# Kernel tuning notes

Measured on AMD Instinct MI355X. Metric: run time of the kernel, lower is better.

Reference implementation:

```python
import jax, jax.numpy as jnp
import numpy as np

B_, L_, DM = 64, 2048, 12
DI, DS, DC, DTR = 24, 16, 4, 1  # d_inner=expand*d_model, d_state, d_conv, dt_rank=ceil(12/16)


def _ln(x, g, b, eps=1e-12):
    m = x.mean(-1, keepdims=True)
    v = ((x - m) ** 2).mean(-1, keepdims=True)
    return (x - m) / jnp.sqrt(v + eps) * g + b


def setup_inputs() -> dict:
    key = jax.random.key(0)
    ks = jax.random.split(key, 16)
    r = lambda k, s, sc=0.1: jax.random.normal(k, s, jnp.float32) * sc
    A = jnp.tile(jnp.arange(1, DS + 1, dtype=jnp.float32), (DI, 1))  # standard S4D-real init
    return {
        "x": jax.random.normal(ks[0], (B_, L_, DM), jnp.float32),
        "in_proj_w": r(ks[1], (2 * DI, DM)),
        "conv_w": r(ks[2], (DI, 1, DC)),
        "conv_b": r(ks[3], (DI,)),
        "x_proj_w": r(ks[4], (DTR + 2 * DS, DI)),
        "dt_w": r(ks[5], (DI, DTR)),
        "dt_b": r(ks[6], (DI,)),
        "A_log": jnp.log(A),
        "Dp": r(ks[7], (DI,)) + 1.0,
        "out_proj_w": r(ks[8], (DM, DI)),
        "ln1_g": jnp.ones(DM, jnp.float32), "ln1_b": jnp.zeros(DM, jnp.float32),
        "ffn_w1": r(ks[9], (4 * DM, DM)), "ffn_b1": jnp.zeros(4 * DM, jnp.float32),
        "ffn_w2": r(ks[10], (DM, 4 * DM)), "ffn_b2": jnp.zeros(DM, jnp.float32),
        "ffn_ln_g": jnp.ones(DM, jnp.float32), "ffn_ln_b": jnp.zeros(DM, jnp.float32),
        "cnn_w": r(ks[11], (DM, DM, 3)), "cnn_b": r(ks[12], (DM,)),
        "lin1_w": r(ks[13], (12, 24)), "lin1_b": jnp.zeros(12, jnp.float32),
        "lin2_w": r(ks[14], (20, 12)), "lin2_b": jnp.zeros(20, jnp.float32),
        "lin3_w": r(ks[15], (1, 20)), "lin3_b": jnp.zeros(1, jnp.float32),
    }


def reference(x, in_proj_w, conv_w, conv_b, x_proj_w, dt_w, dt_b, A_log, Dp,
              out_proj_w, ln1_g, ln1_b, ffn_w1, ffn_b1, ffn_w2, ffn_b2,
              ffn_ln_g, ffn_ln_b, cnn_w, cnn_b, lin1_w, lin1_b,
              lin2_w, lin2_b, lin3_w, lin3_b):
    Bsz = x.shape[0]
    # ---- Mamba block ----
    xz = jnp.einsum('bld,ed->ble', x, in_proj_w)            # [B,L,2*DI]
    xi, z = xz[..., :DI], xz[..., DI:]
    xc = jax.lax.conv_general_dilated(
        xi.transpose(0, 2, 1), conv_w, (1,), [(DC - 1, 0)],
        dimension_numbers=('NCH', 'OIH', 'NCH'), feature_group_count=DI)
    xi = jax.nn.silu(xc.transpose(0, 2, 1) + conv_b)        # causal depthwise conv + SiLU
    xdb = jnp.einsum('bld,ed->ble', xi, x_proj_w)           # [B,L,dt_rank+2*DS]
    dt, Bm, Cm = xdb[..., :DTR], xdb[..., DTR:DTR + DS], xdb[..., DTR + DS:]
    delta = jax.nn.softplus(jnp.einsum('blr,dr->bld', dt, dt_w) + dt_b)  # [B,L,DI]
    A = -jnp.exp(A_log)                                     # [DI,DS]
    dA = jnp.exp(delta[..., None] * A)                      # [B,L,DI,DS]
    dBx = delta[..., None] * Bm[:, :, None, :] * xi[..., None]

    def step(h, inp):
        a, bx, c = inp
        h = a * h + bx                                      # [B,DI,DS]
        return h, jnp.einsum('bdn,bn->bd', h, c)

    h0 = jnp.zeros((Bsz, DI, DS), x.dtype)
    _, ys = jax.lax.scan(step, h0, (dA.transpose(1, 0, 2, 3),
                                    dBx.transpose(1, 0, 2, 3),
                                    Cm.transpose(1, 0, 2)))
    y = ys.transpose(1, 0, 2) + xi * Dp                     # skip D*x
    y = y * jax.nn.silu(z)
    m_out = jnp.einsum('ble,de->bld', y, out_proj_w)        # [B,L,DM]
    h = _ln(m_out, ln1_g, ln1_b)                            # num_layers==1: no residual
    # ---- FeedForward (with residual + LN) ----
    ff = jax.nn.gelu(jnp.einsum('bld,ed->ble', h, ffn_w1) + ffn_b1, approximate=False)
    ff = jnp.einsum('ble,de->bld', ff, ffn_w2) + ffn_b2
    x_mamba = _ln(ff + h, ffn_ln_g, ffn_ln_b)
    # ---- FFT magnitude + Conv1d path (padding=1 to keep length L; see notes) ----
    xf = jnp.abs(jnp.fft.fft(x, axis=1)).astype(x.dtype)
    xcnn = jax.lax.conv_general_dilated(
        xf.transpose(0, 2, 1), cnn_w, (1,), [(1, 1)],
        dimension_numbers=('NCH', 'OIH', 'NCH')) + cnn_b[None, :, None]
    xcnn = xcnn.transpose(0, 2, 1)                          # [B,L,12]
    # ---- fusion head ----
    comb = jnp.concatenate([x_mamba, xcnn], axis=-1)        # [B,L,24]
    o = jax.nn.elu(jnp.einsum('ble,de->bld', comb, lin1_w) + lin1_b)
    o = jnp.einsum('bld,ed->ble', o, lin2_w) + lin2_b
    o = jnp.einsum('ble,oe->blo', o, lin3_w) + lin3_b       # [B,L,1]
    return jax.nn.sigmoid(o.mean(axis=1)).squeeze()          # [B]
```

## Files before the change

### kernel.cpp

```cpp
#include <hip/hip_runtime.h>
#include <math.h>

#define B_  64
#define L_  2048
#define DM  12
#define DI  24
#define DS  16
#define DC  4
#define DTR 1
#define T_  (B_ * L_)
#define NCHUNK 128
#define CHUNK  16


__device__ __forceinline__ float siluf(float v)  { return v / (1.0f + __expf(-v)); }
__device__ __forceinline__ float eluf(float v) { return v > 0.0f ? v : __expf(v) - 1.0f; }

__device__ __forceinline__ float fast_erff(float x) {
    const float ax = fabsf(x);
    const float t  = 1.0f / fmaf(0.3275911f, ax, 1.0f);
    float p = fmaf(1.061405429f, t, -1.453152027f);
    p = fmaf(p, t, 1.421413741f);
    p = fmaf(p, t, -0.284496736f);
    p = fmaf(p, t, 0.254829592f);
    p *= t;
    const float r = 1.0f - p * __expf(-ax * ax);
    return copysignf(r, x);
}
__device__ __forceinline__ float geluf(float v) {
    return 0.5f * v * (1.0f + fast_erff(v * 0.70710678118654752440f));
}

__global__ __launch_bounds__(256) void k_proj_fft(
    const float* __restrict__ x, const float* __restrict__ w_in,
    const float* __restrict__ conv_w, const float* __restrict__ conv_b,
    const float* __restrict__ xproj_w,
    float* __restrict__ xi_out, float* __restrict__ zs_out,
    float* __restrict__ dt_out, float* __restrict__ Bm_out,
    float* __restrict__ Cm_out, float* __restrict__ xfT)
{
    __shared__ float smem[12620];
    const int tid = threadIdx.x;

    if (blockIdx.x < 512) {
        float* s_st = smem + 6476;
        const int b   = blockIdx.x >> 3;
        const int l0  = (blockIdx.x & 7) << 8;
        const int l   = l0 + tid;
        const int t   = b * L_ + l;
        const size_t t0 = (size_t)b * L_ + l0;

        float xv[DM];
        *(float4*)&xv[0] = *(const float4*)&x[t * DM + 0];
        *(float4*)&xv[4] = *(const float4*)&x[t * DM + 4];
        *(float4*)&xv[8] = *(const float4*)&x[t * DM + 8];

        float zsv[DI];
#pragma unroll
        for (int e = 0; e < DI; ++e) {
            float acc = 0.0f, accz = 0.0f;
#pragma unroll
            for (int d = 0; d < DM; ++d) {
                acc  += xv[d] * w_in[e * DM + d];
                accz += xv[d] * w_in[(DI + e) * DM + d];
            }
            smem[(tid + 3) * 25 + e] = acc;
            zsv[e] = siluf(accz);
        }
        if (tid < 3) {
            const int lh = l0 - 3 + tid;
            if (lh < 0) {
                for (int e = 0; e < DI; ++e) smem[tid * 25 + e] = 0.0f;
            } else {
                const int th = b * L_ + lh;
                float xh[DM];
                for (int d = 0; d < DM; ++d) xh[d] = x[th * DM + d];
                for (int e = 0; e < DI; ++e) {
                    float acc = 0.0f;
                    for (int d = 0; d < DM; ++d) acc += xh[d] * w_in[e * DM + d];
                    smem[tid * 25 + e] = acc;
                }
            }
        }
#pragma unroll
        for (int e = 0; e < DI; ++e) s_st[tid * DI + e] = zsv[e];
        __syncthreads();
        {
            float4* g = (float4*)(zs_out + t0 * DI);
            const float4* s4 = (const float4*)s_st;
#pragma unroll
            for (int k = 0; k < 6; ++k) g[k * 256 + tid] = s4[k * 256 + tid];
        }

        float xi[DI];
#pragma unroll
        for (int dch = 0; dch < DI; ++dch) {
            float acc = conv_b[dch];
#pragma unroll
            for (int k = 0; k < DC; ++k)
                acc += smem[(tid + k) * 25 + dch] * conv_w[dch * DC + k];
            xi[dch] = siluf(acc);
        }
        float dt = 0.0f;
#pragma unroll
        for (int d = 0; d < DI; ++d) dt += xi[d] * xproj_w[d];
        dt_out[t] = dt;
        float Bv[DS], Cv[DS];
#pragma unroll
        for (int e = 0; e < DS; ++e) {
            float accB = 0.0f, accC = 0.0f;
#pragma unroll
            for (int d = 0; d < DI; ++d) {
                accB += xi[d] * xproj_w[(1 + e) * DI + d];
                accC += xi[d] * xproj_w[(1 + DS + e) * DI + d];
            }
            Bv[e] = accB;
            Cv[e] = accC;
        }

        __syncthreads();
#pragma unroll
        for (int e = 0; e < DI; ++e) s_st[tid * DI + e] = xi[e];
        __syncthreads();
        {
            float4* g = (float4*)(xi_out + t0 * DI);
            const float4* s4 = (const float4*)s_st;
#pragma unroll
            for (int k = 0; k < 6; ++k) g[k * 256 + tid] = s4[k * 256 + tid];
        }
        __syncthreads();
#pragma unroll
        for (int e = 0; e < DS; ++e) s_st[tid * DS + e] = Bv[e];
        __syncthreads();
        {
            float4* g = (float4*)(Bm_out + t0 * DS);
            const float4* s4 = (const float4*)s_st;
#pragma unroll
            for (int k = 0; k < 4; ++k) g[k * 256 + tid] = s4[k * 256 + tid];
        }
        __syncthreads();
#pragma unroll
        for (int e = 0; e < DS; ++e) s_st[tid * DS + e] = Cv[e];
        __syncthreads();
        {
            float4* g = (float4*)(Cm_out + t0 * DS);
            const float4* s4 = (const float4*)s_st;
#pragma unroll
            for (int k = 0; k < 4; ++k) g[k * 256 + tid] = s4[k * 256 + tid];
        }
    } else {
        float* re  = smem;
        float* im  = smem + 2048;
        float* twr = smem + 4096;
        float* twi = smem + 5120;
        const int bid = blockIdx.x - 512;
        const int b   = bid / (DM / 2);
        const int p   = bid % (DM / 2);
        for (int j = tid; j < 1024; j += 256) {
            const float ang = -6.283185307179586f * (float)j * (1.0f / 2048.0f);
            float s, c;
            sincosf(ang, &s, &c);
            twr[j] = c; twi[j] = s;
        }
        for (int i = tid; i < 2048; i += 256) {
            const int r = (int)(__brev((unsigned)i) >> 21);
            const float2 v = *(const float2*)&x[(size_t)(b * L_ + i) * DM + 2 * p];
            re[r] = v.x;
            im[r] = v.y;
        }
        __syncthreads();
        for (int s = 1; s <= 11; ++s) {
            const int half  = 1 << (s - 1);
            const int tstep = 2048 >> s;
            for (int i = tid; i < 1024; i += 256) {
                const int j   = i & (half - 1);
                const int grp = i >> (s - 1);
                const int pos = (grp << s) + j;
                const float wr = twr[j * tstep], wi = twi[j * tstep];
                const float ar = re[pos + half], ai = im[pos + half];
                const float vr = wr * ar - wi * ai;
                const float vi = wr * ai + wi * ar;
                const float ur = re[pos], ui = im[pos];
                re[pos] = ur + vr;          im[pos] = ui + vi;
                re[pos + half] = ur - vr;   im[pos + half] = ui - vi;
            }
            __syncthreads();
        }
        float* row1 = xfT + (size_t)(b * DM + 2 * p) * L_;
        float* row2 = row1 + L_;
        for (int k = tid; k < 2048; k += 256) {
            const int nk = (2048 - k) & 2047;
            const float zr = re[k],  zi = im[k];
            const float qr = re[nk], qi = im[nk];
            const float e1r = zr + qr, e1i = zi - qi;
            const float e2r = zr - qr, e2i = zi + qi;
            row1[k] = 0.5f * sqrtf(e1r * e1r + e1i * e1i);
            row2[k] = 0.5f * sqrtf(e2r * e2r + e2i * e2i);
        }
    }
}

__global__ __launch_bounds__(384) void k_scan1(
    const float* __restrict__ dt_in, const float* __restrict__ xi,
    const float* __restrict__ Bm, const float* __restrict__ A_log,
    const float* __restrict__ dt_w, const float* __restrict__ dt_b,
    float* __restrict__ Sd, float* __restrict__ H)
{
    const int tid = threadIdx.x;
    const int d   = tid % DI;
    const int cl  = tid / DI;
    const int b   = blockIdx.x >> 3;
    const int c   = ((blockIdx.x & 7) << 4) + cl;
    const int t0  = b * L_ + c * CHUNK;

    float An[DS];
#pragma unroll
    for (int j = 0; j < DS; ++j) An[j] = -__expf(A_log[d * DS + j]);
    const float dtw = dt_w[d], dtb = dt_b[d];

    float h[DS];
#pragma unroll
    for (int j = 0; j < DS; ++j) h[j] = 0.0f;
    float sumdel = 0.0f;

    const float*  pDt = dt_in + t0;
    const float*  pX  = xi + (size_t)t0 * DI + d;
    const float4* pB  = (const float4*)(Bm + (size_t)t0 * DS);

#pragma unroll 4
    for (int i = 0; i < CHUNK; ++i) {
        const float v = fmaf(pDt[i], dtw, dtb);
        const float e = __expf(v);
        const float delta = (v > 20.0f) ? v : __logf(1.0f + e);
        const float u = delta * pX[i * DI];
        sumdel += delta;
        const float4 B0 = pB[i * 4 + 0];
        const float4 B1 = pB[i * 4 + 1];
        const float4 B2 = pB[i * 4 + 2];
        const float4 B3 = pB[i * 4 + 3];
#pragma unroll
        for (int j = 0; j < DS; ++j) {
            const float a = __expf(delta * An[j]);
            h[j] = a * h[j] + u * ((j < 4) ? (&B0.x)[j] : (j < 8) ? (&B1.x)[j - 4]
                                   : (j < 12) ? (&B2.x)[j - 8] : (&B3.x)[j - 12]);
        }
    }
    const int cu = (b * DI + d) * NCHUNK + c;
    Sd[cu] = sumdel;
    float4* pH = (float4*)(H + (size_t)cu * DS);
    pH[0] = make_float4(h[0], h[1], h[2], h[3]);
    pH[1] = make_float4(h[4], h[5], h[6], h[7]);
    pH[2] = make_float4(h[8], h[9], h[10], h[11]);
    pH[3] = make_float4(h[12], h[13], h[14], h[15]);
}

__global__ __launch_bounds__(256) void k_scan2(
    const float* __restrict__ Sd, float* __restrict__ H,
    const float* __restrict__ A_log)
{
    const int idx  = blockIdx.x * 256 + threadIdx.x;
    const int n    = idx & 15;
    const int rest = idx >> 4;
    const int d    = rest % DI;
    const float An = -__expf(A_log[d * DS + n]);
    float Hc = 0.0f;
    const int base = rest * NCHUNK;
    for (int cg = 0; cg < NCHUNK / 8; ++cg) {
        float sd[8], hh[8];
#pragma unroll
        for (int k = 0; k < 8; ++k) {
            sd[k] = Sd[base + cg * 8 + k];
            hh[k] = H[(base + cg * 8 + k) * DS + n];
        }
        float aa[8];
#pragma unroll
        for (int k = 0; k < 8; ++k) aa[k] = __expf(An * sd[k]);
#pragma unroll
        for (int k = 0; k < 8; ++k) {
            H[(base + cg * 8 + k) * DS + n] = Hc;
            Hc = aa[k] * Hc + hh[k];
        }
    }
}

__global__ __launch_bounds__(384) void k_scan3(
    const float* __restrict__ dt_in, const float* __restrict__ xi,
    const float* __restrict__ Bm, const float* __restrict__ Cm,
    const float* __restrict__ zs, const float* __restrict__ Dp,
    const float* __restrict__ H0, const float* __restrict__ A_log,
    const float* __restrict__ dt_w, const float* __restrict__ dt_b,
    float* __restrict__ y_out)
{
    const int tid = threadIdx.x;
    const int d   = tid % DI;
    const int cl  = tid / DI;
    const int b   = blockIdx.x >> 3;
    const int c   = ((blockIdx.x & 7) << 4) + cl;
    const int t0  = b * L_ + c * CHUNK;

    float An[DS];
#pragma unroll
    for (int j = 0; j < DS; ++j) An[j] = -__expf(A_log[d * DS + j]);
    const float dtw = dt_w[d], dtb = dt_b[d];
    const float Dpd = Dp[d];

    const int cu = (b * DI + d) * NCHUNK + c;
    float h[DS];
    {
        const float4* pH0 = (const float4*)(H0 + (size_t)cu * DS);
        const float4 a0 = pH0[0], a1 = pH0[1], a2 = pH0[2], a3 = pH0[3];
        h[0]=a0.x; h[1]=a0.y; h[2]=a0.z; h[3]=a0.w;
        h[4]=a1.x; h[5]=a1.y; h[6]=a1.z; h[7]=a1.w;
        h[8]=a2.x; h[9]=a2.y; h[10]=a2.z; h[11]=a2.w;
        h[12]=a3.x; h[13]=a3.y; h[14]=a3.z; h[15]=a3.w;
    }

    const float*  pDt = dt_in + t0;
    const float*  pX  = xi + (size_t)t0 * DI + d;
    const float*  pZ  = zs + (size_t)t0 * DI + d;
    const float4* pB  = (const float4*)(Bm + (size_t)t0 * DS);
    const float4* pC  = (const float4*)(Cm + (size_t)t0 * DS);
    float*        pY  = y_out + (size_t)t0 * DI + d;

#pragma unroll 4
    for (int i = 0; i < CHUNK; ++i) {
        const float v = fmaf(pDt[i], dtw, dtb);
        const float e = __expf(v);
        const float delta = (v > 20.0f) ? v : __logf(1.0f + e);
        const float xiv = pX[i * DI];
        const float u = delta * xiv;
        const float4 B0 = pB[i * 4 + 0];
        const float4 B1 = pB[i * 4 + 1];
        const float4 B2 = pB[i * 4 + 2];
        const float4 B3 = pB[i * 4 + 3];
        const float4 C0 = pC[i * 4 + 0];
        const float4 C1 = pC[i * 4 + 1];
        const float4 C2 = pC[i * 4 + 2];
        const float4 C3 = pC[i * 4 + 3];
        float p = 0.0f;
#pragma unroll
        for (int j = 0; j < DS; ++j) {
            const float a = __expf(delta * An[j]);
            const float Bj = (j < 4) ? (&B0.x)[j] : (j < 8) ? (&B1.x)[j - 4]
                             : (j < 12) ? (&B2.x)[j - 8] : (&B3.x)[j - 12];
            const float Cj = (j < 4) ? (&C0.x)[j] : (j < 8) ? (&C1.x)[j - 4]
                             : (j < 12) ? (&C2.x)[j - 8] : (&C3.x)[j - 12];
            h[j] = a * h[j] + u * Bj;
            p += h[j] * Cj;
        }
        pY[i * DI] = (p + xiv * Dpd) * pZ[i * DI];
    }
}

__global__ __launch_bounds__(256, 2) void k_tail(
    const float* __restrict__ yg, const float* __restrict__ xfT,
    const float* __restrict__ out_w,
    const float* __restrict__ ln1_g, const float* __restrict__ ln1_b,
    const float* __restrict__ w1, const float* __restrict__ b1,
    const float* __restrict__ w2, const float* __restrict__ b2,
    const float* __restrict__ lng, const float* __restrict__ lnb,
    const float* __restrict__ cnn_w, const float* __restrict__ cnn_b,
    const float* __restrict__ l1w, const float* __restrict__ l1b,
    const float* __restrict__ l2w, const float* __restrict__ l2b,
    const float* __restrict__ l3w,
    float* __restrict__ part)
{
    __shared__ float sV[DM];
    __shared__ float sC0;
    __shared__ float sred[256];

    const int tid = threadIdx.x;
    const int b   = blockIdx.x >> 3;
    const int l   = ((blockIdx.x & 7) << 8) + tid;
    const int t   = b * L_ + l;

    float y[DI];
#pragma unroll
    for (int e = 0; e < DI; ++e) y[e] = yg[(size_t)t * DI + e];
    float xfm[DM], xf0[DM], xfp[DM];
#pragma unroll
    for (int i = 0; i < DM; ++i) {
        const float* row = xfT + (size_t)(b * DM + i) * L_;
        xfm[i] = (l == 0)      ? 0.0f : row[l - 1];
        xf0[i] = row[l];
        xfp[i] = (l == L_ - 1) ? 0.0f : row[l + 1];
    }

    if (tid < DM) {
        float acc = 0.0f;
#pragma unroll
        for (int e = 0; e < 20; ++e) acc += l3w[e] * l2w[e * DM + tid];
        sV[tid] = acc;
    }
    if (tid == DM) {
        float c = 0.0f;
#pragma unroll
        for (int e = 0; e < 20; ++e) c += l2b[e] * l3w[e];
        sC0 = c;
    }
    __syncthreads();

    float m[DM];
#pragma unroll
    for (int j = 0; j < DM; ++j) {
        float acc = 0.0f;
#pragma unroll
        for (int e = 0; e < DI; ++e) acc += y[e] * out_w[j * DI + e];
        m[j] = acc;
    }
    float mean = 0.0f;
#pragma unroll
    for (int j = 0; j < DM; ++j) mean += m[j];
    mean *= (1.0f / DM);
    float var = 0.0f;
#pragma unroll
    for (int j = 0; j < DM; ++j) { const float dv = m[j] - mean; var += dv * dv; }
    var *= (1.0f / DM);
    const float inv1 = rsqrtf(var + 1e-12f);
    float h[DM];
#pragma unroll
    for (int j = 0; j < DM; ++j) h[j] = (m[j] - mean) * inv1 * ln1_g[j] + ln1_b[j];

    float ff[4 * DM];
#pragma unroll
    for (int e = 0; e < 4 * DM; ++e) {
        float acc = b1[e];
#pragma unroll
        for (int j = 0; j < DM; ++j) acc += h[j] * w1[e * DM + j];
        ff[e] = geluf(acc);
    }
    float f2[DM];
#pragma unroll
    for (int j = 0; j < DM; ++j) {
        float acc = b2[j];
#pragma unroll
        for (int e = 0; e < 4 * DM; ++e) acc += ff[e] * w2[j * (4 * DM) + e];
        f2[j] = acc + h[j];
    }
    mean = 0.0f;
#pragma unroll
    for (int j = 0; j < DM; ++j) mean += f2[j];
    mean *= (1.0f / DM);
    var = 0.0f;
#pragma unroll
    for (int j = 0; j < DM; ++j) { const float dv = f2[j] - mean; var += dv * dv; }
    var *= (1.0f / DM);
    const float inv2 = rsqrtf(var + 1e-12f);
    float xm[DM];
#pragma unroll
    for (int j = 0; j < DM; ++j) xm[j] = (f2[j] - mean) * inv2 * lng[j] + lnb[j];

    float xc[DM];
#pragma unroll
    for (int o = 0; o < DM; ++o) {
        float acc = cnn_b[o];
#pragma unroll
        for (int i = 0; i < DM; ++i) {
            const int wb = (o * DM + i) * 3;
            acc += xfm[i] * cnn_w[wb] + xf0[i] * cnn_w[wb + 1] + xfp[i] * cnn_w[wb + 2];
        }
        xc[o] = acc;
    }

    float o3 = sC0;
#pragma unroll
    for (int d = 0; d < DM; ++d) {
        float acc = l1b[d];
#pragma unroll
        for (int e = 0; e < DM; ++e) acc += xm[e] * l1w[d * (2 * DM) + e];
#pragma unroll
        for (int e = 0; e < DM; ++e) acc += xc[e] * l1w[d * (2 * DM) + DM + e];
        o3 += eluf(acc) * sV[d];
    }

    sred[tid] = o3;
    __syncthreads();
    for (int s = 128; s > 0; s >>= 1) {
        if (tid < s) sred[tid] += sred[tid + s];
        __syncthreads();
    }
    if (tid == 0) part[blockIdx.x] = sred[0];
}

__global__ void k_final(const float* __restrict__ part, const float* __restrict__ l3b,
                        float* __restrict__ out)
{
    const int b = threadIdx.x;
    if (b < B_) {
        float s = 0.0f;
        for (int i = 0; i < 8; ++i) s += part[b * 8 + i];
        s = s * (1.0f / (float)L_) + l3b[0];
        out[b] = 1.0f / (1.0f + __expf(-s));
    }
}

extern "C" void kernel_launch(void* const* d_in, const int* in_sizes, int n_in,
                              void* d_out, int out_size, void* d_ws, size_t ws_size,
                              hipStream_t stream)
{
    const float* x        = (const float*)d_in[0];
    const float* in_w     = (const float*)d_in[1];
    const float* conv_w   = (const float*)d_in[2];
    const float* conv_b   = (const float*)d_in[3];
    const float* xproj_w  = (const float*)d_in[4];
    const float* dt_w     = (const float*)d_in[5];
    const float* dt_b     = (const float*)d_in[6];
    const float* A_log    = (const float*)d_in[7];
    const float* Dp       = (const float*)d_in[8];
    const float* out_w    = (const float*)d_in[9];
    const float* ln1_g    = (const float*)d_in[10];
    const float* ln1_b    = (const float*)d_in[11];
    const float* ffn_w1   = (const float*)d_in[12];
    const float* ffn_b1   = (const float*)d_in[13];
    const float* ffn_w2   = (const float*)d_in[14];
    const float* ffn_b2   = (const float*)d_in[15];
    const float* ffn_ln_g = (const float*)d_in[16];
    const float* ffn_ln_b = (const float*)d_in[17];
    const float* cnn_w    = (const float*)d_in[18];
    const float* cnn_b    = (const float*)d_in[19];
    const float* l1w      = (const float*)d_in[20];
    const float* l1b      = (const float*)d_in[21];
    const float* l2w      = (const float*)d_in[22];
    const float* l2b      = (const float*)d_in[23];
    const float* l3w      = (const float*)d_in[24];
    const float* l3b      = (const float*)d_in[25];
    float* out = (float*)d_out;

    float* ws = (float*)d_ws;
    const size_t nTDI = (size_t)T_ * DI;
    const size_t nTDS = (size_t)T_ * DS;
    const size_t nCH  = (size_t)B_ * DI * NCHUNK;
    float* w_xi   = ws;
    float* w_zs   = w_xi + nTDI;
    float* w_y    = w_zs + nTDI;
    float* w_dt   = w_y + nTDI;
    float* w_Bm   = w_dt + T_;
    float* w_Cm   = w_Bm + nTDS;
    float* w_Sd   = w_Cm + nTDS;
    float* w_H    = w_Sd + nCH;
    float* w_xf   = w_H + nCH * DS;
    float* w_part = w_xf + (size_t)B_ * DM * L_;

    k_proj_fft<<<512 + B_ * (DM / 2), 256, 0, stream>>>(
        x, in_w, conv_w, conv_b, xproj_w,
        w_xi, w_zs, w_dt, w_Bm, w_Cm, w_xf);
    k_scan1<<<B_ * (NCHUNK / 16), 384, 0, stream>>>(w_dt, w_xi, w_Bm, A_log,
                                                    dt_w, dt_b, w_Sd, w_H);
    k_scan2<<<96, 256, 0, stream>>>(w_Sd, w_H, A_log);
    k_scan3<<<B_ * (NCHUNK / 16), 384, 0, stream>>>(w_dt, w_xi, w_Bm, w_Cm, w_zs, Dp,
                                                    w_H, A_log, dt_w, dt_b, w_y);
    k_tail<<<512, 256, 0, stream>>>(w_y, w_xf, out_w,
                                    ln1_g, ln1_b, ffn_w1, ffn_b1, ffn_w2, ffn_b2,
                                    ffn_ln_g, ffn_ln_b, cnn_w, cnn_b,
                                    l1w, l1b, l2w, l2b, l3w, w_part);
    k_final<<<1, 64, 0, stream>>>(w_part, l3b, out);
}
```

Baseline: 147.4 us.

## Fuse scan phase 3 with tail MLP head via shared-memory y tile

Merges the final scan pass and the per-token tail network into one kernel. Scan outputs for 256 tokens are staged in shared memory instead of being written to and re-read from global memory, and one kernel launch is removed. In exchange, only 256 of the 384 threads run the heavy tail math. The block now holds a 25 KB shared tile and carries the register pressure of both stages, which may reduce occupancy.

```diff
diff --git a/kernel.cpp b/kernel.cpp
--- a/kernel.cpp
+++ b/kernel.cpp
@@ -283,78 +283,13 @@
     }
 }
 
-__global__ __launch_bounds__(384) void k_scan3(
+__global__ __launch_bounds__(384) void k_scan3_tail(
     const float* __restrict__ dt_in, const float* __restrict__ xi,
     const float* __restrict__ Bm, const float* __restrict__ Cm,
     const float* __restrict__ zs, const float* __restrict__ Dp,
     const float* __restrict__ H0, const float* __restrict__ A_log,
     const float* __restrict__ dt_w, const float* __restrict__ dt_b,
-    float* __restrict__ y_out)
-{
-    const int tid = threadIdx.x;
-    const int d   = tid % DI;
-    const int cl  = tid / DI;
-    const int b   = blockIdx.x >> 3;
-    const int c   = ((blockIdx.x & 7) << 4) + cl;
-    const int t0  = b * L_ + c * CHUNK;
-
-    float An[DS];
-#pragma unroll
-    for (int j = 0; j < DS; ++j) An[j] = -__expf(A_log[d * DS + j]);
-    const float dtw = dt_w[d], dtb = dt_b[d];
-    const float Dpd = Dp[d];
-
-    const int cu = (b * DI + d) * NCHUNK + c;
-    float h[DS];
-    {
-        const float4* pH0 = (const float4*)(H0 + (size_t)cu * DS);
-        const float4 a0 = pH0[0], a1 = pH0[1], a2 = pH0[2], a3 = pH0[3];
-        h[0]=a0.x; h[1]=a0.y; h[2]=a0.z; h[3]=a0.w;
-        h[4]=a1.x; h[5]=a1.y; h[6]=a1.z; h[7]=a1.w;
-        h[8]=a2.x; h[9]=a2.y; h[10]=a2.z; h[11]=a2.w;
-        h[12]=a3.x; h[13]=a3.y; h[14]=a3.z; h[15]=a3.w;
-    }
-
-    const float*  pDt = dt_in + t0;
-    const float*  pX  = xi + (size_t)t0 * DI + d;
-    const float*  pZ  = zs + (size_t)t0 * DI + d;
-    const float4* pB  = (const float4*)(Bm + (size_t)t0 * DS);
-    const float4* pC  = (const float4*)(Cm + (size_t)t0 * DS);
-    float*        pY  = y_out + (size_t)t0 * DI + d;
-
-#pragma unroll 4
-    for (int i = 0; i < CHUNK; ++i) {
-        const float v = fmaf(pDt[i], dtw, dtb);
-        const float e = __expf(v);
-        const float delta = (v > 20.0f) ? v : __logf(1.0f + e);
-        const float xiv = pX[i * DI];
-        const float u = delta * xiv;
-        const float4 B0 = pB[i * 4 + 0];
-        const float4 B1 = pB[i * 4 + 1];
-        const float4 B2 = pB[i * 4 + 2];
-        const float4 B3 = pB[i * 4 + 3];
-        const float4 C0 = pC[i * 4 + 0];
-        const float4 C1 = pC[i * 4 + 1];
-        const float4 C2 = pC[i * 4 + 2];
-        const float4 C3 = pC[i * 4 + 3];
-        float p = 0.0f;
-#pragma unroll
-        for (int j = 0; j < DS; ++j) {
-            const float a = __expf(delta * An[j]);
-            const float Bj = (j < 4) ? (&B0.x)[j] : (j < 8) ? (&B1.x)[j - 4]
-                             : (j < 12) ? (&B2.x)[j - 8] : (&B3.x)[j - 12];
-            const float Cj = (j < 4) ? (&C0.x)[j] : (j < 8) ? (&C1.x)[j - 4]
-                             : (j < 12) ? (&C2.x)[j - 8] : (&C3.x)[j - 12];
-            h[j] = a * h[j] + u * Bj;
-            p += h[j] * Cj;
-        }
-        pY[i * DI] = (p + xiv * Dpd) * pZ[i * DI];
-    }
-}
-
-__global__ __launch_bounds__(256, 2) void k_tail(
-    const float* __restrict__ yg, const float* __restrict__ xfT,
-    const float* __restrict__ out_w,
+    const float* __restrict__ xfT, const float* __restrict__ out_w,
     const float* __restrict__ ln1_g, const float* __restrict__ ln1_b,
     const float* __restrict__ w1, const float* __restrict__ b1,
     const float* __restrict__ w2, const float* __restrict__ b2,
@@ -365,25 +300,70 @@
     const float* __restrict__ l3w,
     float* __restrict__ part)
 {
+    __shared__ float s_y[256][25];
     __shared__ float sV[DM];
     __shared__ float sC0;
-    __shared__ float sred[256];
+    __shared__ float sred[512];
 
     const int tid = threadIdx.x;
+    const int d   = tid % DI;
+    const int cl  = tid / DI;
     const int b   = blockIdx.x >> 3;
-    const int l   = ((blockIdx.x & 7) << 8) + tid;
-    const int t   = b * L_ + l;
-
-    float y[DI];
-#pragma unroll
-    for (int e = 0; e < DI; ++e) y[e] = yg[(size_t)t * DI + e];
-    float xfm[DM], xf0[DM], xfp[DM];
-#pragma unroll
-    for (int i = 0; i < DM; ++i) {
-        const float* row = xfT + (size_t)(b * DM + i) * L_;
-        xfm[i] = (l == 0)      ? 0.0f : row[l - 1];
-        xf0[i] = row[l];
-        xfp[i] = (l == L_ - 1) ? 0.0f : row[l + 1];
+    const int c   = ((blockIdx.x & 7) << 4) + cl;
+    const int t0  = b * L_ + c * CHUNK;
+
+    {
+        float An[DS];
+#pragma unroll
+        for (int j = 0; j < DS; ++j) An[j] = -__expf(A_log[d * DS + j]);
+        const float dtw = dt_w[d], dtb = dt_b[d];
+        const float Dpd = Dp[d];
+
+        const int cu = (b * DI + d) * NCHUNK + c;
+        float h[DS];
+        {
+            const float4* pH0 = (const float4*)(H0 + (size_t)cu * DS);
+            const float4 a0 = pH0[0], a1 = pH0[1], a2 = pH0[2], a3 = pH0[3];
+            h[0]=a0.x; h[1]=a0.y; h[2]=a0.z; h[3]=a0.w;
+            h[4]=a1.x; h[5]=a1.y; h[6]=a1.z; h[7]=a1.w;
+            h[8]=a2.x; h[9]=a2.y; h[10]=a2.z; h[11]=a2.w;
+            h[12]=a3.x; h[13]=a3.y; h[14]=a3.z; h[15]=a3.w;
+        }
+
+        const float*  pDt = dt_in + t0;
+        const float*  pX  = xi + (size_t)t0 * DI + d;
+        const float*  pZ  = zs + (size_t)t0 * DI + d;
+        const float4* pB  = (const float4*)(Bm + (size_t)t0 * DS);
+        const float4* pC  = (const float4*)(Cm + (size_t)t0 * DS);
+
+#pragma unroll 4
+        for (int i = 0; i < CHUNK; ++i) {
+            const float v = fmaf(pDt[i], dtw, dtb);
+            const float e = __expf(v);
+            const float delta = (v > 20.0f) ? v : __logf(1.0f + e);
+            const float xiv = pX[i * DI];
+            const float u = delta * xiv;
+            const float4 B0 = pB[i * 4 + 0];
+            const float4 B1 = pB[i * 4 + 1];
+            const float4 B2 = pB[i * 4 + 2];
+            const float4 B3 = pB[i * 4 + 3];
+            const float4 C0 = pC[i * 4 + 0];
+            const float4 C1 = pC[i * 4 + 1];
+            const float4 C2 = pC[i * 4 + 2];
+            const float4 C3 = pC[i * 4 + 3];
+            float p = 0.0f;
+#pragma unroll
+            for (int j = 0; j < DS; ++j) {
+                const float a = __expf(delta * An[j]);
+                const float Bj = (j < 4) ? (&B0.x)[j] : (j < 8) ? (&B1.x)[j - 4]
+                                 : (j < 12) ? (&B2.x)[j - 8] : (&B3.x)[j - 12];
+                const float Cj = (j < 4) ? (&C0.x)[j] : (j < 8) ? (&C1.x)[j - 4]
+                                 : (j < 12) ? (&C2.x)[j - 8] : (&C3.x)[j - 12];
+                h[j] = a * h[j] + u * Bj;
+                p += h[j] * Cj;
+            }
+            s_y[cl * CHUNK + i][d] = (p + xiv * Dpd) * pZ[i * DI];
+        }
     }
 
     if (tid < DM) {
@@ -393,89 +373,108 @@
         sV[tid] = acc;
     }
     if (tid == DM) {
-        float c = 0.0f;
-#pragma unroll
-        for (int e = 0; e < 20; ++e) c += l2b[e] * l3w[e];
-        sC0 = c;
+        float cc = 0.0f;
+#pragma unroll
+        for (int e = 0; e < 20; ++e) cc += l2b[e] * l3w[e];
+        sC0 = cc;
     }
     __syncthreads();
 
-    float m[DM];
-#pragma unroll
-    for (int j = 0; j < DM; ++j) {
-        float acc = 0.0f;
-#pragma unroll
-        for (int e = 0; e < DI; ++e) acc += y[e] * out_w[j * DI + e];
-        m[j] = acc;
-    }
-    float mean = 0.0f;
-#pragma unroll
-    for (int j = 0; j < DM; ++j) mean += m[j];
-    mean *= (1.0f / DM);
-    float var = 0.0f;
-#pragma unroll
-    for (int j = 0; j < DM; ++j) { const float dv = m[j] - mean; var += dv * dv; }
-    var *= (1.0f / DM);
-    const float inv1 = rsqrtf(var + 1e-12f);
-    float h[DM];
-#pragma unroll
-    for (int j = 0; j < DM; ++j) h[j] = (m[j] - mean) * inv1 * ln1_g[j] + ln1_b[j];
-
-    float ff[4 * DM];
-#pragma unroll
-    for (int e = 0; e < 4 * DM; ++e) {
-        float acc = b1[e];
-#pragma unroll
-        for (int j = 0; j < DM; ++j) acc += h[j] * w1[e * DM + j];
-        ff[e] = geluf(acc);
-    }
-    float f2[DM];
-#pragma unroll
-    for (int j = 0; j < DM; ++j) {
-        float acc = b2[j];
-#pragma unroll
-        for (int e = 0; e < 4 * DM; ++e) acc += ff[e] * w2[j * (4 * DM) + e];
-        f2[j] = acc + h[j];
-    }
-    mean = 0.0f;
-#pragma unroll
-    for (int j = 0; j < DM; ++j) mean += f2[j];
-    mean *= (1.0f / DM);
-    var = 0.0f;
-#pragma unroll
-    for (int j = 0; j < DM; ++j) { const float dv = f2[j] - mean; var += dv * dv; }
-    var *= (1.0f / DM);
-    const float inv2 = rsqrtf(var + 1e-12f);
-    float xm[DM];
-#pragma unroll
-    for (int j = 0; j < DM; ++j) xm[j] = (f2[j] - mean) * inv2 * lng[j] + lnb[j];
-
-    float xc[DM];
-#pragma unroll
-    for (int o = 0; o < DM; ++o) {
-        float acc = cnn_b[o];
+    float o3 = 0.0f;
+    if (tid < 256) {
+        const int tok = tid;
+        const int l   = ((blockIdx.x & 7) << 8) + tok;
+
+        float y[DI];
+#pragma unroll
+        for (int e = 0; e < DI; ++e) y[e] = s_y[tok][e];
+        float xfm[DM], xf0[DM], xfp[DM];
 #pragma unroll
         for (int i = 0; i < DM; ++i) {
-            const int wb = (o * DM + i) * 3;
-            acc += xfm[i] * cnn_w[wb] + xf0[i] * cnn_w[wb + 1] + xfp[i] * cnn_w[wb + 2];
-        }
-        xc[o] = acc;
-    }
-
-    float o3 = sC0;
-#pragma unroll
-    for (int d = 0; d < DM; ++d) {
-        float acc = l1b[d];
-#pragma unroll
-        for (int e = 0; e < DM; ++e) acc += xm[e] * l1w[d * (2 * DM) + e];
-#pragma unroll
-        for (int e = 0; e < DM; ++e) acc += xc[e] * l1w[d * (2 * DM) + DM + e];
-        o3 += eluf(acc) * sV[d];
+            const float* row = xfT + (size_t)(b * DM + i) * L_;
+            xfm[i] = (l == 0)      ? 0.0f : row[l - 1];
+            xf0[i] = row[l];
+            xfp[i] = (l == L_ - 1) ? 0.0f : row[l + 1];
+        }
+
+        float m[DM];
+#pragma unroll
+        for (int j = 0; j < DM; ++j) {
+            float acc = 0.0f;
+#pragma unroll
+            for (int e = 0; e < DI; ++e) acc += y[e] * out_w[j * DI + e];
+            m[j] = acc;
+        }
+        float mean = 0.0f;
+#pragma unroll
+        for (int j = 0; j < DM; ++j) mean += m[j];
+        mean *= (1.0f / DM);
+        float var = 0.0f;
+#pragma unroll
+        for (int j = 0; j < DM; ++j) { const float dv = m[j] - mean; var += dv * dv; }
+        var *= (1.0f / DM);
+        const float inv1 = rsqrtf(var + 1e-12f);
+        float h[DM];
+#pragma unroll
+        for (int j = 0; j < DM; ++j) h[j] = (m[j] - mean) * inv1 * ln1_g[j] + ln1_b[j];
+
+        float ff[4 * DM];
+#pragma unroll
+        for (int e = 0; e < 4 * DM; ++e) {
+            float acc = b1[e];
+#pragma unroll
+            for (int j = 0; j < DM; ++j) acc += h[j] * w1[e * DM + j];
+            ff[e] = geluf(acc);
+        }
+        float f2[DM];
+#pragma unroll
+        for (int j = 0; j < DM; ++j) {
+            float acc = b2[j];
+#pragma unroll
+            for (int e = 0; e < 4 * DM; ++e) acc += ff[e] * w2[j * (4 * DM) + e];
+            f2[j] = acc + h[j];
+        }
+        mean = 0.0f;
+#pragma unroll
+        for (int j = 0; j < DM; ++j) mean += f2[j];
+        mean *= (1.0f / DM);
+        var = 0.0f;
+#pragma unroll
+        for (int j = 0; j < DM; ++j) { const float dv = f2[j] - mean; var += dv * dv; }
+        var *= (1.0f / DM);
+        const float inv2 = rsqrtf(var + 1e-12f);
+        float xm[DM];
+#pragma unroll
+        for (int j = 0; j < DM; ++j) xm[j] = (f2[j] - mean) * inv2 * lng[j] + lnb[j];
+
+        float xc[DM];
+#pragma unroll
+        for (int o = 0; o < DM; ++o) {
+            float acc = cnn_b[o];
+#pragma unroll
+            for (int i = 0; i < DM; ++i) {
+                const int wb = (o * DM + i) * 3;
+                acc += xfm[i] * cnn_w[wb] + xf0[i] * cnn_w[wb + 1] + xfp[i] * cnn_w[wb + 2];
+            }
+            xc[o] = acc;
+        }
+
+        o3 = sC0;
+#pragma unroll
+        for (int dd = 0; dd < DM; ++dd) {
+            float acc = l1b[dd];
+#pragma unroll
+            for (int e = 0; e < DM; ++e) acc += xm[e] * l1w[dd * (2 * DM) + e];
+#pragma unroll
+            for (int e = 0; e < DM; ++e) acc += xc[e] * l1w[dd * (2 * DM) + DM + e];
+            o3 += eluf(acc) * sV[dd];
+        }
     }
 
     sred[tid] = o3;
+    if (tid < 128) sred[384 + tid] = 0.0f;
     __syncthreads();
-    for (int s = 128; s > 0; s >>= 1) {
+    for (int s = 256; s > 0; s >>= 1) {
         if (tid < s) sred[tid] += sred[tid + s];
         __syncthreads();
     }
@@ -540,6 +539,7 @@
     float* w_H    = w_Sd + nCH;
     float* w_xf   = w_H + nCH * DS;
     float* w_part = w_xf + (size_t)B_ * DM * L_;
+    (void)w_y;
 
     k_proj_fft<<<512 + B_ * (DM / 2), 256, 0, stream>>>(
         x, in_w, conv_w, conv_b, xproj_w,
@@ -547,11 +547,9 @@
     k_scan1<<<B_ * (NCHUNK / 16), 384, 0, stream>>>(w_dt, w_xi, w_Bm, A_log,
                                                     dt_w, dt_b, w_Sd, w_H);
     k_scan2<<<96, 256, 0, stream>>>(w_Sd, w_H, A_log);
-    k_scan3<<<B_ * (NCHUNK / 16), 384, 0, stream>>>(w_dt, w_xi, w_Bm, w_Cm, w_zs, Dp,
-                                                    w_H, A_log, dt_w, dt_b, w_y);
-    k_tail<<<512, 256, 0, stream>>>(w_y, w_xf, out_w,
-                                    ln1_g, ln1_b, ffn_w1, ffn_b1, ffn_w2, ffn_b2,
-                                    ffn_ln_g, ffn_ln_b, cnn_w, cnn_b,
-                                    l1w, l1b, l2w, l2b, l3w, w_part);
+    k_scan3_tail<<<B_ * (NCHUNK / 16), 384, 0, stream>>>(
+        w_dt, w_xi, w_Bm, w_Cm, w_zs, Dp, w_H, A_log, dt_w, dt_b,
+        w_xf, out_w, ln1_g, ln1_b, ffn_w1, ffn_b1, ffn_w2, ffn_b2,
+        ffn_ln_g, ffn_ln_b, cnn_w, cnn_b, l1w, l1b, l2w, l2b, l3w, w_part);
     k_final<<<1, 64, 0, stream>>>(w_part, l3b, out);
 }
```

Result: slower. 158.7 us (+7.7%).

## Split scan state dimension across thread pairs with DPP reduction

Applied to the files above, without the earlier changes.

The chunked selective-scan kernels (scan1 and scan3) now give each (chunk, channel) pair two threads, each owning 8 of the 16 state elements. Twice as many blocks are launched, which raises parallelism and occupancy and cuts per-thread register use. In scan3 the partial C·h dot products are combined across the lane pair with a DPP swap-add. The cost is that softplus(delta) is computed twice, the dt and x loads are duplicated, and half the lanes sit idle on the output store.

```diff
diff --git a/kernel.cpp b/kernel.cpp
--- a/kernel.cpp
+++ b/kernel.cpp
@@ -30,6 +30,9 @@
 __device__ __forceinline__ float geluf(float v) {
     return 0.5f * v * (1.0f + fast_erff(v * 0.70710678118654752440f));
 }
+
+#define DPP_ADD(p, ctrl) \
+    (p) += __int_as_float(__builtin_amdgcn_update_dpp(0, __float_as_int(p), (ctrl), 0xF, 0xF, true))
 
 __global__ __launch_bounds__(256) void k_proj_fft(
     const float* __restrict__ x, const float* __restrict__ w_in,
@@ -207,20 +210,21 @@
     float* __restrict__ Sd, float* __restrict__ H)
 {
     const int tid = threadIdx.x;
-    const int d   = tid % DI;
-    const int cl  = tid / DI;
-    const int b   = blockIdx.x >> 3;
-    const int c   = ((blockIdx.x & 7) << 4) + cl;
+    const int q   = tid & 1;
+    const int d   = (tid >> 1) % DI;
+    const int cl  = tid / (2 * DI);
+    const int b   = blockIdx.x >> 4;
+    const int c   = ((blockIdx.x & 15) << 3) + cl;
     const int t0  = b * L_ + c * CHUNK;
 
-    float An[DS];
-#pragma unroll
-    for (int j = 0; j < DS; ++j) An[j] = -__expf(A_log[d * DS + j]);
+    float An[8];
+#pragma unroll
+    for (int j = 0; j < 8; ++j) An[j] = -__expf(A_log[d * DS + q * 8 + j]);
     const float dtw = dt_w[d], dtb = dt_b[d];
 
-    float h[DS];
-#pragma unroll
-    for (int j = 0; j < DS; ++j) h[j] = 0.0f;
+    float h[8];
+#pragma unroll
+    for (int j = 0; j < 8; ++j) h[j] = 0.0f;
     float sumdel = 0.0f;
 
     const float*  pDt = dt_in + t0;
@@ -234,24 +238,19 @@
         const float delta = (v > 20.0f) ? v : __logf(1.0f + e);
         const float u = delta * pX[i * DI];
         sumdel += delta;
-        const float4 B0 = pB[i * 4 + 0];
-        const float4 B1 = pB[i * 4 + 1];
-        const float4 B2 = pB[i * 4 + 2];
-        const float4 B3 = pB[i * 4 + 3];
-#pragma unroll
-        for (int j = 0; j < DS; ++j) {
+        const float4 B0 = pB[i * 4 + q * 2];
+        const float4 B1 = pB[i * 4 + q * 2 + 1];
+#pragma unroll
+        for (int j = 0; j < 8; ++j) {
             const float a = __expf(delta * An[j]);
-            h[j] = a * h[j] + u * ((j < 4) ? (&B0.x)[j] : (j < 8) ? (&B1.x)[j - 4]
-                                   : (j < 12) ? (&B2.x)[j - 8] : (&B3.x)[j - 12]);
+            h[j] = a * h[j] + u * ((j < 4) ? (&B0.x)[j] : (&B1.x)[j - 4]);
         }
     }
     const int cu = (b * DI + d) * NCHUNK + c;
-    Sd[cu] = sumdel;
-    float4* pH = (float4*)(H + (size_t)cu * DS);
+    if (q == 0) Sd[cu] = sumdel;
+    float4* pH = (float4*)(H + (size_t)cu * DS + q * 8);
     pH[0] = make_float4(h[0], h[1], h[2], h[3]);
     pH[1] = make_float4(h[4], h[5], h[6], h[7]);
-    pH[2] = make_float4(h[8], h[9], h[10], h[11]);
-    pH[3] = make_float4(h[12], h[13], h[14], h[15]);
 }
 
 __global__ __launch_bounds__(256) void k_scan2(
@@ -292,27 +291,26 @@
     float* __restrict__ y_out)
 {
     const int tid = threadIdx.x;
-    const int d   = tid % DI;
-    const int cl  = tid / DI;
-    const int b   = blockIdx.x >> 3;
-    const int c   = ((blockIdx.x & 7) << 4) + cl;
+    const int q   = tid & 1;
+    const int d   = (tid >> 1) % DI;
+    const int cl  = tid / (2 * DI);
+    const int b   = blockIdx.x >> 4;
+    const int c   = ((blockIdx.x & 15) << 3) + cl;
     const int t0  = b * L_ + c * CHUNK;
 
-    float An[DS];
-#pragma unroll
-    for (int j = 0; j < DS; ++j) An[j] = -__expf(A_log[d * DS + j]);
+    float An[8];
+#pragma unroll
+    for (int j = 0; j < 8; ++j) An[j] = -__expf(A_log[d * DS + q * 8 + j]);
     const float dtw = dt_w[d], dtb = dt_b[d];
     const float Dpd = Dp[d];
 
     const int cu = (b * DI + d) * NCHUNK + c;
-    float h[DS];
+    float h[8];
     {
-        const float4* pH0 = (const float4*)(H0 + (size_t)cu * DS);
-        const float4 a0 = pH0[0], a1 = pH0[1], a2 = pH0[2], a3 = pH0[3];
+        const float4* pH0 = (const float4*)(H0 + (size_t)cu * DS + q * 8);
+        const float4 a0 = pH0[0], a1 = pH0[1];
         h[0]=a0.x; h[1]=a0.y; h[2]=a0.z; h[3]=a0.w;
         h[4]=a1.x; h[5]=a1.y; h[6]=a1.z; h[7]=a1.w;
-        h[8]=a2.x; h[9]=a2.y; h[10]=a2.z; h[11]=a2.w;
-        h[12]=a3.x; h[13]=a3.y; h[14]=a3.z; h[15]=a3.w;
     }
 
     const float*  pDt = dt_in + t0;
@@ -329,26 +327,21 @@
         const float delta = (v > 20.0f) ? v : __logf(1.0f + e);
         const float xiv = pX[i * DI];
         const float u = delta * xiv;
-        const float4 B0 = pB[i * 4 + 0];
-        const float4 B1 = pB[i * 4 + 1];
-        const float4 B2 = pB[i * 4 + 2];
-        const float4 B3 = pB[i * 4 + 3];
-        const float4 C0 = pC[i * 4 + 0];
-        const float4 C1 = pC[i * 4 + 1];
-        const float4 C2 = pC[i * 4 + 2];
-        const float4 C3 = pC[i * 4 + 3];
+        const float4 B0 = pB[i * 4 + q * 2];
+        const float4 B1 = pB[i * 4 + q * 2 + 1];
+        const float4 C0 = pC[i * 4 + q * 2];
+        const float4 C1 = pC[i * 4 + q * 2 + 1];
         float p = 0.0f;
 #pragma unroll
-        for (int j = 0; j < DS; ++j) {
+        for (int j = 0; j < 8; ++j) {
             const float a = __expf(delta * An[j]);
-            const float Bj = (j < 4) ? (&B0.x)[j] : (j < 8) ? (&B1.x)[j - 4]
-                             : (j < 12) ? (&B2.x)[j - 8] : (&B3.x)[j - 12];
-            const float Cj = (j < 4) ? (&C0.x)[j] : (j < 8) ? (&C1.x)[j - 4]
-                             : (j < 12) ? (&C2.x)[j - 8] : (&C3.x)[j - 12];
+            const float Bj = (j < 4) ? (&B0.x)[j] : (&B1.x)[j - 4];
+            const float Cj = (j < 4) ? (&C0.x)[j] : (&C1.x)[j - 4];
             h[j] = a * h[j] + u * Bj;
             p += h[j] * Cj;
         }
-        pY[i * DI] = (p + xiv * Dpd) * pZ[i * DI];
+        DPP_ADD(p, 0xB1);
+        if (q == 0) pY[i * DI] = (p + xiv * Dpd) * pZ[i * DI];
     }
 }
 
@@ -544,11 +537,11 @@
     k_proj_fft<<<512 + B_ * (DM / 2), 256, 0, stream>>>(
         x, in_w, conv_w, conv_b, xproj_w,
         w_xi, w_zs, w_dt, w_Bm, w_Cm, w_xf);
-    k_scan1<<<B_ * (NCHUNK / 16), 384, 0, stream>>>(w_dt, w_xi, w_Bm, A_log,
-                                                    dt_w, dt_b, w_Sd, w_H);
+    k_scan1<<<B_ * (NCHUNK / 8), 384, 0, stream>>>(w_dt, w_xi, w_Bm, A_log,
+                                                   dt_w, dt_b, w_Sd, w_H);
     k_scan2<<<96, 256, 0, stream>>>(w_Sd, w_H, A_log);
-    k_scan3<<<B_ * (NCHUNK / 16), 384, 0, stream>>>(w_dt, w_xi, w_Bm, w_Cm, w_zs, Dp,
-                                                    w_H, A_log, dt_w, dt_b, w_y);
+    k_scan3<<<B_ * (NCHUNK / 8), 384, 0, stream>>>(w_dt, w_xi, w_Bm, w_Cm, w_zs, Dp,
+                                                   w_H, A_log, dt_w, dt_b, w_y);
     k_tail<<<512, 256, 0, stream>>>(w_y, w_xf, out_w,
                                     ln1_g, ln1_b, ffn_w1, ffn_b1, ffn_w2, ffn_b2,
                                     ffn_ln_g, ffn_ln_b, cnn_w, cnn_b,
```

After: 142.9 us, median of 4. -3.1%, faster.
